# Kernel optimization log

Measured on AMD Instinct MI355X. Metric: run time of the kernel, lower is better.

## Reference

```python
import jax, jax.numpy as jnp
import numpy as np

NUM_HEADS = 8
HEAD_DIM = 64


def setup_inputs() -> dict:
    key = jax.random.key(0)
    k1, k2, k3 = jax.random.split(key, 3)
    B, T, S, D = 2, 32, 1024, 512
    inner = NUM_HEADS * HEAD_DIM  # 512
    x = jax.random.normal(k1, (B, T, S, D), dtype=jnp.float32)
    W_qkv = jax.random.normal(k2, (D, 3 * inner), dtype=jnp.float32) * (D ** -0.5)
    W_out = jax.random.normal(k3, (inner, D), dtype=jnp.float32) * (inner ** -0.5)
    return {"x": x, "W_qkv": W_qkv, "W_out": W_out}


def reference(x, W_qkv, W_out):
    # x: (B, T, S, D); causal attention over T at each spatial position S.
    B, T, S, D = x.shape
    H, hd = NUM_HEADS, HEAD_DIM
    scale = hd ** -0.5
    qkv = jnp.einsum('btsd,de->btse', x, W_qkv)  # (B,T,S,3*H*hd)
    qkv = qkv.reshape(B, T, S, 3, H, hd)
    q, k, v = qkv[..., 0, :, :], qkv[..., 1, :, :], qkv[..., 2, :, :]  # (B,T,S,H,hd)
    # attention logits per (batch, spatial, head): (B,S,H,Tq,Tk)
    attn = jnp.einsum('bqshd,bkshd->bshqk', q, k) * scale
    causal_mask = jnp.triu(jnp.ones((T, T), dtype=bool), 1)  # True above diagonal
    attn = jnp.where(causal_mask, -jnp.inf, attn)
    attn = jax.nn.softmax(attn, axis=-1)
    out = jnp.einsum('bshqk,bkshd->bqshd', attn, v)  # (B,T,S,H,hd)
    out = out.reshape(B, T, S, H * hd)
    return jnp.einsum('btse,ed->btsd', out, W_out)  # (B,T,S,D)
```

## Files before the change

### kernel.cpp

```cpp
#include <hip/hip_runtime.h>
#include <cstdint>
#include <cstddef>

#define KDIM 512

typedef __attribute__((ext_vector_type(8))) __bf16 bf16x8;
typedef __attribute__((ext_vector_type(8))) unsigned short ushort8;
typedef __attribute__((ext_vector_type(4))) float f32x4;
typedef unsigned short u16;

__device__ __forceinline__ float bf2f(u16 u) {
  union { unsigned u32; float f; } x; x.u32 = ((unsigned)u) << 16; return x.f;
}
__device__ __forceinline__ u16 f2bf(float f) {
  union { float f; unsigned u; } x; x.f = f;
  unsigned u = x.u;
  unsigned r = (u + 0x7fffu + ((u >> 16) & 1u)) >> 16;
  return (u16)r;
}

__global__ __launch_bounds__(256) void cast_x_kernel(const float* __restrict__ in,
                                                     u16* __restrict__ out, int n4) {
  int i = blockIdx.x * 256 + threadIdx.x;
  if (i >= n4) return;
  float4 v = ((const float4*)in)[i];
  ushort4 o;
  o.x = f2bf(v.x); o.y = f2bf(v.y); o.z = f2bf(v.z); o.w = f2bf(v.w);
  ((ushort4*)out)[i] = o;
}

__global__ __launch_bounds__(256) void transpose_cast_kernel(const float* __restrict__ in,
                                                             u16* __restrict__ out,
                                                             int R, int C) {
  int o = blockIdx.x * 256 + threadIdx.x;
  if (o >= R * C) return;
  int r = o % R;
  int c = o / R;
  out[o] = f2bf(in[(size_t)r * C + c]);
}

__device__ __forceinline__ void gload_lds16(const void* g, void* l) {
  __builtin_amdgcn_global_load_lds((__attribute__((address_space(1))) unsigned int*)g,
                                   (__attribute__((address_space(3))) unsigned int*)l,
                                   16, 0, 0);
}

template <typename OutT>
__global__ __launch_bounds__(512, 2) void gemm256_kernel(const u16* __restrict__ A,
                                                         const u16* __restrict__ Bt,
                                                         OutT* __restrict__ C,
                                                         int N, int NXT) {
  __shared__ __attribute__((aligned(16))) u16 As[4][8192];
  __shared__ __attribute__((aligned(16))) u16 Bs[4][8192];
  const int tid = threadIdx.x;
  const int wid = tid >> 6, l = tid & 63;
  const int wm = wid >> 2, wn = wid & 3;
  const int g = l >> 4, i = l & 15;

  const int nwg = gridDim.x;
  const int cpx = nwg >> 3;
  const int bid = blockIdx.x;
  const int swz = (bid & 7) * cpx + (bid >> 3);
  const int mt = swz / NXT, nt = swz % NXT;
  const size_t m0 = (size_t)mt * 256, n0 = (size_t)nt * 256;

  const int srow = tid >> 2;
  const int sbp = tid & 3;
  const int sbs = sbp ^ ((srow >> 1) & 3);

  f32x4 acc[8][4] = {};

  auto STAGE = [&](int t, int slot) {
    const int k0 = t << 5;
    gload_lds16(A + (m0 + srow) * KDIM + k0 + sbs * 8, &As[slot][tid * 8]);
    gload_lds16(A + (m0 + 128 + srow) * KDIM + k0 + sbs * 8, &As[slot][(tid + 512) * 8]);
    gload_lds16(Bt + (n0 + srow) * KDIM + k0 + sbs * 8, &Bs[slot][tid * 8]);
    gload_lds16(Bt + (n0 + 128 + srow) * KDIM + k0 + sbs * 8, &Bs[slot][(tid + 512) * 8]);
  };

  auto COMPUTE = [&](int slot) {
    bf16x8 af[8], bv[4];
#pragma unroll
    for (int m = 0; m < 8; ++m) {
      int row = wm * 128 + m * 16 + i;
      af[m] = *(const bf16x8*)&As[slot][row * 32 + ((g ^ ((row >> 1) & 3)) << 3)];
    }
#pragma unroll
    for (int n = 0; n < 4; ++n) {
      int row = wn * 64 + n * 16 + i;
      bv[n] = *(const bf16x8*)&Bs[slot][row * 32 + ((g ^ ((row >> 1) & 3)) << 3)];
    }
    __builtin_amdgcn_s_setprio(1);
#pragma unroll
    for (int m = 0; m < 8; ++m)
#pragma unroll
      for (int n = 0; n < 4; ++n)
        acc[m][n] = __builtin_amdgcn_mfma_f32_16x16x32_bf16(af[m], bv[n], acc[m][n], 0, 0, 0);
    __builtin_amdgcn_s_setprio(0);
  };

  STAGE(0, 0);
  STAGE(1, 1);
  STAGE(2, 2);
  for (int t = 0; t < 14; ++t) {
    asm volatile("s_waitcnt vmcnt(8)" ::: "memory");
    __builtin_amdgcn_s_barrier();
    __builtin_amdgcn_sched_barrier(0);
    if (t < 13) STAGE(t + 3, (t + 3) & 3);
    COMPUTE(t & 3);
    __builtin_amdgcn_sched_barrier(0);
  }
  asm volatile("s_waitcnt vmcnt(4)" ::: "memory");
  __builtin_amdgcn_s_barrier();
  __builtin_amdgcn_sched_barrier(0);
  COMPUTE(2);
  __builtin_amdgcn_sched_barrier(0);
  asm volatile("s_waitcnt vmcnt(0)" ::: "memory");
  __builtin_amdgcn_s_barrier();
  __builtin_amdgcn_sched_barrier(0);
  COMPUTE(3);

#pragma unroll
  for (int m = 0; m < 8; ++m) {
    size_t rowb = m0 + wm * 128 + m * 16 + g * 4;
#pragma unroll
    for (int n = 0; n < 4; ++n) {
      size_t colg = n0 + wn * 64 + n * 16 + i;
#pragma unroll
      for (int r = 0; r < 4; ++r) {
        size_t idx = (rowb + r) * (size_t)N + colg;
        if constexpr (sizeof(OutT) == 2) C[idx] = (OutT)f2bf(acc[m][n][r]);
        else C[idx] = acc[m][n][r];
      }
    }
  }
}

__global__ __launch_bounds__(256, 4) void attn_mfma_kernel(const u16* __restrict__ qkv,
                                                           u16* __restrict__ out) {
  const int bs = blockIdx.x >> 1;
  const int hg = blockIdx.x & 1;
  const int b = bs >> 10, s = bs & 1023;
  __shared__ __attribute__((aligned(16))) u16 Ks[4][2048];
  __shared__ __attribute__((aligned(16))) u16 Vt[4][2048];
  __shared__ __attribute__((aligned(16))) u16 Ps[4][1024];

  const int tid = threadIdx.x;
  const int wv = tid >> 6;
  const int h = hg * 4 + wv;
  const int l = tid & 63;
  const int g = l >> 4, i = l & 15;

  const size_t tstride = (size_t)1024 * 1536;
  const size_t base = ((size_t)(b * 32) * 1024 + s) * 1536;

  {
    const int krow = l >> 3;
    const int dbs = (l & 7) ^ krow;
#pragma unroll
    for (int j = 0; j < 4; ++j) {
      int k = j * 8 + krow;
      gload_lds16(qkv + base + (size_t)k * tstride + 512 + h * 64 + dbs * 8, &Ks[wv][j * 512]);
    }
  }

  const int vk = l & 31;
  ushort8 vv[4];
#pragma unroll
  for (int j = 0; j < 4; ++j) {
    int c = (l >> 5) + 2 * j;
    vv[j] = *(const ushort8*)(qkv + base + (size_t)vk * tstride + 1024 + h * 64 + c * 8);
  }

  bf16x8 bq[2][2];
#pragma unroll
  for (int n = 0; n < 2; ++n)
#pragma unroll
    for (int ks = 0; ks < 2; ++ks)
      bq[n][ks] = *(const bf16x8*)(qkv + base + (size_t)(n * 16 + i) * tstride + h * 64 + ks * 32 + g * 8);

#pragma unroll
  for (int j = 0; j < 4; ++j) {
    int c = (l >> 5) + 2 * j;
#pragma unroll
    for (int u = 0; u < 8; ++u) {
      int d = c * 8 + u;
      int pos = (vk >> 3) ^ (d & 3);
      Vt[wv][d * 32 + pos * 8 + (vk & 7)] = vv[j][u];
    }
  }

  asm volatile("s_waitcnt vmcnt(0)" ::: "memory");

  f32x4 sc[2][2] = {};
#pragma unroll
  for (int m = 0; m < 2; ++m)
#pragma unroll
    for (int ks = 0; ks < 2; ++ks) {
      int k = m * 16 + i;
      int pos = (ks * 4 + g) ^ (k & 7);
      bf16x8 ak = *(const bf16x8*)&Ks[wv][k * 64 + pos * 8];
      sc[m][0] = __builtin_amdgcn_mfma_f32_16x16x32_bf16(ak, bq[0][ks], sc[m][0], 0, 0, 0);
      sc[m][1] = __builtin_amdgcn_mfma_f32_16x16x32_bf16(ak, bq[1][ks], sc[m][1], 0, 0, 0);
    }

  float p[2][2][4];
#pragma unroll
  for (int n = 0; n < 2; ++n) {
    int q = n * 16 + i;
    float m0 = -1e30f;
#pragma unroll
    for (int m = 0; m < 2; ++m)
#pragma unroll
      for (int r = 0; r < 4; ++r) {
        int k = m * 16 + g * 4 + r;
        float v = (k <= q) ? sc[m][n][r] * 0.125f : -1e30f;
        p[m][n][r] = v;
        m0 = fmaxf(m0, v);
      }
    m0 = fmaxf(m0, __shfl_xor(m0, 16));
    m0 = fmaxf(m0, __shfl_xor(m0, 32));
    float s0 = 0.f;
#pragma unroll
    for (int m = 0; m < 2; ++m)
#pragma unroll
      for (int r = 0; r < 4; ++r) {
        float e = __expf(p[m][n][r] - m0);
        p[m][n][r] = e;
        s0 += e;
      }
    s0 += __shfl_xor(s0, 16);
    s0 += __shfl_xor(s0, 32);
    float inv = 1.f / s0;
#pragma unroll
    for (int m = 0; m < 2; ++m)
#pragma unroll
      for (int r = 0; r < 4; ++r) p[m][n][r] *= inv;
  }

#pragma unroll
  for (int m = 0; m < 2; ++m)
#pragma unroll
    for (int n = 0; n < 2; ++n) {
      int q = n * 16 + i;
      int kb = m * 2 + (g >> 1);
      int pos = kb ^ (q & 3);
      uint2 wo;
      wo.x = (unsigned)f2bf(p[m][n][0]) | ((unsigned)f2bf(p[m][n][1]) << 16);
      wo.y = (unsigned)f2bf(p[m][n][2]) | ((unsigned)f2bf(p[m][n][3]) << 16);
      *(uint2*)&Ps[wv][q * 32 + pos * 8 + (g & 1) * 4] = wo;
    }

  asm volatile("s_waitcnt lgkmcnt(0)" ::: "memory");

  bf16x8 bv[4];
#pragma unroll
  for (int np = 0; np < 4; ++np) {
    int d = np * 16 + i;
    int pos = g ^ (d & 3);
    bv[np] = *(const bf16x8*)&Vt[wv][d * 32 + pos * 8];
  }
  f32x4 o[2][4] = {};
#pragma unroll
  for (int mp = 0; mp < 2; ++mp) {
    int q = mp * 16 + i;
    int pos = g ^ (q & 3);
    bf16x8 ap = *(const bf16x8*)&Ps[wv][q * 32 + pos * 8];
#pragma unroll
    for (int np = 0; np < 4; ++np)
      o[mp][np] = __builtin_amdgcn_mfma_f32_16x16x32_bf16(ap, bv[np], o[mp][np], 0, 0, 0);
  }

#pragma unroll
  for (int mp = 0; mp < 2; ++mp)
#pragma unroll
    for (int r = 0; r < 4; ++r) {
      int q = mp * 16 + g * 4 + r;
      u16* dst = out + ((size_t)((b * 32 + q) * 1024 + s)) * 512 + h * 64;
#pragma unroll
      for (int np = 0; np < 4; ++np)
        dst[np * 16 + i] = f2bf(o[mp][np][r]);
    }
}

extern "C" void kernel_launch(void* const* d_in, const int* in_sizes, int n_in,
                              void* d_out, int out_size, void* d_ws, size_t ws_size,
                              hipStream_t stream) {
  const float* x = (const float*)d_in[0];
  const float* Wqkv = (const float*)d_in[1];
  const float* Wout = (const float*)d_in[2];
  float* outp = (float*)d_out;

  char* ws = (char*)d_ws;
  u16* x_bf = (u16*)(ws);
  u16* qkv_bf = (u16*)(ws + (size_t)67108864);
  u16* wqkv_t = (u16*)(ws + (size_t)268435456);
  u16* wout_t = (u16*)(ws + (size_t)270008320);
  u16* attn_o = x_bf;

  cast_x_kernel<<<32768, 256, 0, stream>>>(x, x_bf, 8388608);
  transpose_cast_kernel<<<3072, 256, 0, stream>>>(Wqkv, wqkv_t, 512, 1536);
  transpose_cast_kernel<<<1024, 256, 0, stream>>>(Wout, wout_t, 512, 512);

  gemm256_kernel<u16><<<1536, 512, 0, stream>>>(x_bf, wqkv_t, qkv_bf, 1536, 6);

  attn_mfma_kernel<<<4096, 256, 0, stream>>>(qkv_bf, attn_o);

  gemm256_kernel<float><<<512, 512, 0, stream>>>(attn_o, wout_t, outp, 512, 2);
}
```

Measured before the change: 308.8 us.

## Fuse fp32-to-bf16 cast of x into QKV GEMM and retile output GEMM

```diff
diff --git a/kernel.cpp b/kernel.cpp
--- a/kernel.cpp
+++ b/kernel.cpp
@@ -17,16 +17,6 @@
   unsigned u = x.u;
   unsigned r = (u + 0x7fffu + ((u >> 16) & 1u)) >> 16;
   return (u16)r;
-}
-
-__global__ __launch_bounds__(256) void cast_x_kernel(const float* __restrict__ in,
-                                                     u16* __restrict__ out, int n4) {
-  int i = blockIdx.x * 256 + threadIdx.x;
-  if (i >= n4) return;
-  float4 v = ((const float4*)in)[i];
-  ushort4 o;
-  o.x = f2bf(v.x); o.y = f2bf(v.y); o.z = f2bf(v.z); o.w = f2bf(v.w);
-  ((ushort4*)out)[i] = o;
 }
 
 __global__ __launch_bounds__(256) void transpose_cast_kernel(const float* __restrict__ in,
@@ -45,13 +35,12 @@
                                    16, 0, 0);
 }
 
-template <typename OutT>
-__global__ __launch_bounds__(512, 2) void gemm256_kernel(const u16* __restrict__ A,
-                                                         const u16* __restrict__ Bt,
-                                                         OutT* __restrict__ C,
-                                                         int N, int NXT) {
-  __shared__ __attribute__((aligned(16))) u16 As[4][8192];
-  __shared__ __attribute__((aligned(16))) u16 Bs[4][8192];
+__global__ __launch_bounds__(512, 1) void gemm1f_kernel(const float* __restrict__ X,
+                                                        const u16* __restrict__ Bt,
+                                                        u16* __restrict__ C,
+                                                        int N, int NXT) {
+  __shared__ __attribute__((aligned(16))) u16 As[2][8192];
+  __shared__ __attribute__((aligned(16))) u16 Bs[2][8192];
   const int tid = threadIdx.x;
   const int wid = tid >> 6, l = tid & 63;
   const int wm = wid >> 2, wn = wid & 3;
@@ -64,20 +53,38 @@
   const int mt = swz / NXT, nt = swz % NXT;
   const size_t m0 = (size_t)mt * 256, n0 = (size_t)nt * 256;
 
+  const int ar = tid >> 1, ah = tid & 1;
+  const int asw = (ar >> 1) & 3;
   const int srow = tid >> 2;
   const int sbp = tid & 3;
   const int sbs = sbp ^ ((srow >> 1) & 3);
 
   f32x4 acc[8][4] = {};
-
-  auto STAGE = [&](int t, int slot) {
+  float4 av[4];
+
+  auto LOADA = [&](int t) {
+    const float* src = X + (m0 + ar) * KDIM + (t << 5) + ah * 16;
+#pragma unroll
+    for (int j = 0; j < 4; ++j) av[j] = *(const float4*)(src + j * 4);
+  };
+  auto WRITEA = [&](int slot) {
+#pragma unroll
+    for (int jb = 0; jb < 2; ++jb) {
+      ushort8 w;
+#pragma unroll
+      for (int u = 0; u < 4; ++u) {
+        const float4& v = av[jb * 2 + (u >> 1)];
+        w[u * 2 + 0] = f2bf((u & 1) ? v.z : v.x);
+        w[u * 2 + 1] = f2bf((u & 1) ? v.w : v.y);
+      }
+      *(ushort8*)&As[slot][ar * 32 + (((ah * 2 + jb) ^ asw) << 3)] = w;
+    }
+  };
+  auto STAGEB = [&](int t, int slot) {
     const int k0 = t << 5;
-    gload_lds16(A + (m0 + srow) * KDIM + k0 + sbs * 8, &As[slot][tid * 8]);
-    gload_lds16(A + (m0 + 128 + srow) * KDIM + k0 + sbs * 8, &As[slot][(tid + 512) * 8]);
     gload_lds16(Bt + (n0 + srow) * KDIM + k0 + sbs * 8, &Bs[slot][tid * 8]);
     gload_lds16(Bt + (n0 + 128 + srow) * KDIM + k0 + sbs * 8, &Bs[slot][(tid + 512) * 8]);
   };
-
   auto COMPUTE = [&](int slot) {
     bf16x8 af[8], bv[4];
 #pragma unroll
@@ -99,39 +106,114 @@
     __builtin_amdgcn_s_setprio(0);
   };
 
+  LOADA(0);
+  STAGEB(0, 0);
+  asm volatile("s_waitcnt vmcnt(0)" ::: "memory");
+  WRITEA(0);
+  LOADA(1);
+  asm volatile("s_waitcnt lgkmcnt(0)" ::: "memory");
+  __builtin_amdgcn_s_barrier();
+
+  for (int t = 0; t < 16; ++t) {
+    const int buf = t & 1;
+    if (t < 15) STAGEB(t + 1, buf ^ 1);
+    COMPUTE(buf);
+    if (t < 15) {
+      asm volatile("s_waitcnt vmcnt(0)" ::: "memory");
+      WRITEA(buf ^ 1);
+      if (t < 14) LOADA(t + 2);
+      asm volatile("s_waitcnt lgkmcnt(0)" ::: "memory");
+      __builtin_amdgcn_s_barrier();
+    }
+  }
+
+#pragma unroll
+  for (int m = 0; m < 8; ++m) {
+    size_t rowb = m0 + wm * 128 + m * 16 + g * 4;
+#pragma unroll
+    for (int n = 0; n < 4; ++n) {
+      size_t colg = n0 + wn * 64 + n * 16 + i;
+#pragma unroll
+      for (int r = 0; r < 4; ++r)
+        C[(rowb + r) * (size_t)N + colg] = (u16)f2bf(acc[m][n][r]);
+    }
+  }
+}
+
+__global__ __launch_bounds__(256, 4) void gemm128_kernel(const u16* __restrict__ A,
+                                                         const u16* __restrict__ Bt,
+                                                         float* __restrict__ C,
+                                                         int N, int NXT) {
+  __shared__ __attribute__((aligned(16))) u16 As[2][4096];
+  __shared__ __attribute__((aligned(16))) u16 Bs[2][4096];
+  const int tid = threadIdx.x;
+  const int wid = tid >> 6, l = tid & 63;
+  const int wm = wid >> 1, wn = wid & 1;
+  const int g = l >> 4, i = l & 15;
+
+  const int nwg = gridDim.x;
+  const int cpx = nwg >> 3;
+  const int bid = blockIdx.x;
+  const int swz = (bid & 7) * cpx + (bid >> 3);
+  const int mt = swz / NXT, nt = swz % NXT;
+  const size_t m0 = (size_t)mt * 128, n0 = (size_t)nt * 128;
+
+  f32x4 acc[4][4] = {};
+
+  auto STAGE = [&](int t, int slot) {
+    const int k0 = t << 5;
+#pragma unroll
+    for (int c = 0; c < 2; ++c) {
+      int ch = tid + c * 256;
+      int row = ch >> 2;
+      int bbs = (ch & 3) ^ ((row >> 1) & 3);
+      gload_lds16(A + (m0 + row) * KDIM + k0 + bbs * 8, &As[slot][ch * 8]);
+      gload_lds16(Bt + (n0 + row) * KDIM + k0 + bbs * 8, &Bs[slot][ch * 8]);
+    }
+  };
+  auto COMPUTE = [&](int slot) {
+    bf16x8 af[4], bv[4];
+#pragma unroll
+    for (int m = 0; m < 4; ++m) {
+      int row = wm * 64 + m * 16 + i;
+      af[m] = *(const bf16x8*)&As[slot][row * 32 + ((g ^ ((row >> 1) & 3)) << 3)];
+    }
+#pragma unroll
+    for (int n = 0; n < 4; ++n) {
+      int row = wn * 64 + n * 16 + i;
+      bv[n] = *(const bf16x8*)&Bs[slot][row * 32 + ((g ^ ((row >> 1) & 3)) << 3)];
+    }
+    __builtin_amdgcn_s_setprio(1);
+#pragma unroll
+    for (int m = 0; m < 4; ++m)
+#pragma unroll
+      for (int n = 0; n < 4; ++n)
+        acc[m][n] = __builtin_amdgcn_mfma_f32_16x16x32_bf16(af[m], bv[n], acc[m][n], 0, 0, 0);
+    __builtin_amdgcn_s_setprio(0);
+  };
+
   STAGE(0, 0);
-  STAGE(1, 1);
-  STAGE(2, 2);
-  for (int t = 0; t < 14; ++t) {
-    asm volatile("s_waitcnt vmcnt(8)" ::: "memory");
-    __builtin_amdgcn_s_barrier();
-    __builtin_amdgcn_sched_barrier(0);
-    if (t < 13) STAGE(t + 3, (t + 3) & 3);
-    COMPUTE(t & 3);
-    __builtin_amdgcn_sched_barrier(0);
-  }
-  asm volatile("s_waitcnt vmcnt(4)" ::: "memory");
-  __builtin_amdgcn_s_barrier();
-  __builtin_amdgcn_sched_barrier(0);
-  COMPUTE(2);
-  __builtin_amdgcn_sched_barrier(0);
   asm volatile("s_waitcnt vmcnt(0)" ::: "memory");
   __builtin_amdgcn_s_barrier();
-  __builtin_amdgcn_sched_barrier(0);
-  COMPUTE(3);
-
-#pragma unroll
-  for (int m = 0; m < 8; ++m) {
-    size_t rowb = m0 + wm * 128 + m * 16 + g * 4;
+  for (int t = 0; t < 16; ++t) {
+    const int buf = t & 1;
+    if (t < 15) STAGE(t + 1, buf ^ 1);
+    COMPUTE(buf);
+    if (t < 15) {
+      asm volatile("s_waitcnt vmcnt(0)" ::: "memory");
+      __builtin_amdgcn_s_barrier();
+    }
+  }
+
+#pragma unroll
+  for (int m = 0; m < 4; ++m) {
+    size_t rowb = m0 + wm * 64 + m * 16 + g * 4;
 #pragma unroll
     for (int n = 0; n < 4; ++n) {
       size_t colg = n0 + wn * 64 + n * 16 + i;
 #pragma unroll
-      for (int r = 0; r < 4; ++r) {
-        size_t idx = (rowb + r) * (size_t)N + colg;
-        if constexpr (sizeof(OutT) == 2) C[idx] = (OutT)f2bf(acc[m][n][r]);
-        else C[idx] = acc[m][n][r];
-      }
+      for (int r = 0; r < 4; ++r)
+        C[(rowb + r) * (size_t)N + colg] = acc[m][n][r];
     }
   }
 }
@@ -292,19 +374,17 @@
   float* outp = (float*)d_out;
 
   char* ws = (char*)d_ws;
-  u16* x_bf = (u16*)(ws);
+  u16* attn_o = (u16*)(ws);
   u16* qkv_bf = (u16*)(ws + (size_t)67108864);
   u16* wqkv_t = (u16*)(ws + (size_t)268435456);
   u16* wout_t = (u16*)(ws + (size_t)270008320);
-  u16* attn_o = x_bf;
-
-  cast_x_kernel<<<32768, 256, 0, stream>>>(x, x_bf, 8388608);
+
   transpose_cast_kernel<<<3072, 256, 0, stream>>>(Wqkv, wqkv_t, 512, 1536);
   transpose_cast_kernel<<<1024, 256, 0, stream>>>(Wout, wout_t, 512, 512);
 
-  gemm256_kernel<u16><<<1536, 512, 0, stream>>>(x_bf, wqkv_t, qkv_bf, 1536, 6);
+  gemm1f_kernel<<<1536, 512, 0, stream>>>(x, wqkv_t, qkv_bf, 1536, 6);
 
   attn_mfma_kernel<<<4096, 256, 0, stream>>>(qkv_bf, attn_o);
 
-  gemm256_kernel<float><<<512, 512, 0, stream>>>(attn_o, wout_t, outp, 512, 2);
-}
+  gemm128_kernel<<<2048, 256, 0, stream>>>(attn_o, wout_t, outp, 512, 4);
+}
```

Measured after the change: 336.3 us. 1.09x slower.

## Replace 256x256 four-stage GEMM with 128x128 double-buffered GEMM

Applied to the files above, without the earlier changes.

```diff
diff --git a/kernel.cpp b/kernel.cpp
--- a/kernel.cpp
+++ b/kernel.cpp
@@ -46,15 +46,15 @@
 }
 
 template <typename OutT>
-__global__ __launch_bounds__(512, 2) void gemm256_kernel(const u16* __restrict__ A,
+__global__ __launch_bounds__(256, 4) void gemm128_kernel(const u16* __restrict__ A,
                                                          const u16* __restrict__ Bt,
                                                          OutT* __restrict__ C,
                                                          int N, int NXT) {
-  __shared__ __attribute__((aligned(16))) u16 As[4][8192];
-  __shared__ __attribute__((aligned(16))) u16 Bs[4][8192];
+  __shared__ __attribute__((aligned(16))) u16 As[2][4096];
+  __shared__ __attribute__((aligned(16))) u16 Bs[2][4096];
   const int tid = threadIdx.x;
   const int wid = tid >> 6, l = tid & 63;
-  const int wm = wid >> 2, wn = wid & 3;
+  const int wm = wid >> 1, wn = wid & 1;
   const int g = l >> 4, i = l & 15;
 
   const int nwg = gridDim.x;
@@ -62,27 +62,26 @@
   const int bid = blockIdx.x;
   const int swz = (bid & 7) * cpx + (bid >> 3);
   const int mt = swz / NXT, nt = swz % NXT;
-  const size_t m0 = (size_t)mt * 256, n0 = (size_t)nt * 256;
-
-  const int srow = tid >> 2;
-  const int sbp = tid & 3;
-  const int sbs = sbp ^ ((srow >> 1) & 3);
-
-  f32x4 acc[8][4] = {};
+  const size_t m0 = (size_t)mt * 128, n0 = (size_t)nt * 128;
+
+  f32x4 acc[4][4] = {};
 
   auto STAGE = [&](int t, int slot) {
     const int k0 = t << 5;
-    gload_lds16(A + (m0 + srow) * KDIM + k0 + sbs * 8, &As[slot][tid * 8]);
-    gload_lds16(A + (m0 + 128 + srow) * KDIM + k0 + sbs * 8, &As[slot][(tid + 512) * 8]);
-    gload_lds16(Bt + (n0 + srow) * KDIM + k0 + sbs * 8, &Bs[slot][tid * 8]);
-    gload_lds16(Bt + (n0 + 128 + srow) * KDIM + k0 + sbs * 8, &Bs[slot][(tid + 512) * 8]);
+#pragma unroll
+    for (int c = 0; c < 2; ++c) {
+      int ch = tid + c * 256;
+      int row = ch >> 2;
+      int bbs = (ch & 3) ^ ((row >> 1) & 3);
+      gload_lds16(A + (m0 + row) * KDIM + k0 + bbs * 8, &As[slot][ch * 8]);
+      gload_lds16(Bt + (n0 + row) * KDIM + k0 + bbs * 8, &Bs[slot][ch * 8]);
+    }
   };
-
   auto COMPUTE = [&](int slot) {
-    bf16x8 af[8], bv[4];
-#pragma unroll
-    for (int m = 0; m < 8; ++m) {
-      int row = wm * 128 + m * 16 + i;
+    bf16x8 af[4], bv[4];
+#pragma unroll
+    for (int m = 0; m < 4; ++m) {
+      int row = wm * 64 + m * 16 + i;
       af[m] = *(const bf16x8*)&As[slot][row * 32 + ((g ^ ((row >> 1) & 3)) << 3)];
     }
 #pragma unroll
@@ -92,7 +91,7 @@
     }
     __builtin_amdgcn_s_setprio(1);
 #pragma unroll
-    for (int m = 0; m < 8; ++m)
+    for (int m = 0; m < 4; ++m)
 #pragma unroll
       for (int n = 0; n < 4; ++n)
         acc[m][n] = __builtin_amdgcn_mfma_f32_16x16x32_bf16(af[m], bv[n], acc[m][n], 0, 0, 0);
@@ -100,29 +99,21 @@
   };
 
   STAGE(0, 0);
-  STAGE(1, 1);
-  STAGE(2, 2);
-  for (int t = 0; t < 14; ++t) {
-    asm volatile("s_waitcnt vmcnt(8)" ::: "memory");
-    __builtin_amdgcn_s_barrier();
-    __builtin_amdgcn_sched_barrier(0);
-    if (t < 13) STAGE(t + 3, (t + 3) & 3);
-    COMPUTE(t & 3);
-    __builtin_amdgcn_sched_barrier(0);
-  }
-  asm volatile("s_waitcnt vmcnt(4)" ::: "memory");
-  __builtin_amdgcn_s_barrier();
-  __builtin_amdgcn_sched_barrier(0);
-  COMPUTE(2);
-  __builtin_amdgcn_sched_barrier(0);
   asm volatile("s_waitcnt vmcnt(0)" ::: "memory");
   __builtin_amdgcn_s_barrier();
-  __builtin_amdgcn_sched_barrier(0);
-  COMPUTE(3);
-
-#pragma unroll
-  for (int m = 0; m < 8; ++m) {
-    size_t rowb = m0 + wm * 128 + m * 16 + g * 4;
+  for (int t = 0; t < 16; ++t) {
+    const int buf = t & 1;
+    if (t < 15) STAGE(t + 1, buf ^ 1);
+    COMPUTE(buf);
+    if (t < 15) {
+      asm volatile("s_waitcnt vmcnt(0)" ::: "memory");
+      __builtin_amdgcn_s_barrier();
+    }
+  }
+
+#pragma unroll
+  for (int m = 0; m < 4; ++m) {
+    size_t rowb = m0 + wm * 64 + m * 16 + g * 4;
 #pragma unroll
     for (int n = 0; n < 4; ++n) {
       size_t colg = n0 + wn * 64 + n * 16 + i;
@@ -302,9 +293,9 @@
   transpose_cast_kernel<<<3072, 256, 0, stream>>>(Wqkv, wqkv_t, 512, 1536);
   transpose_cast_kernel<<<1024, 256, 0, stream>>>(Wout, wout_t, 512, 512);
 
-  gemm256_kernel<u16><<<1536, 512, 0, stream>>>(x_bf, wqkv_t, qkv_bf, 1536, 6);
+  gemm128_kernel<u16><<<6144, 256, 0, stream>>>(x_bf, wqkv_t, qkv_bf, 1536, 12);
 
   attn_mfma_kernel<<<4096, 256, 0, stream>>>(qkv_bf, attn_o);
 
-  gemm256_kernel<float><<<512, 512, 0, stream>>>(attn_o, wout_t, outp, 512, 2);
-}
+  gemm128_kernel<float><<<2048, 256, 0, stream>>>(attn_o, wout_t, outp, 512, 4);
+}
```

Result: no change. 304.9 us (-1.3%).

## Fuse attention with output projection in one kernel per spatial position

Applied to the files above, without the earlier changes.

```diff
diff --git a/kernel.cpp b/kernel.cpp
--- a/kernel.cpp
+++ b/kernel.cpp
@@ -45,10 +45,9 @@
                                    16, 0, 0);
 }
 
-template <typename OutT>
 __global__ __launch_bounds__(512, 2) void gemm256_kernel(const u16* __restrict__ A,
                                                          const u16* __restrict__ Bt,
-                                                         OutT* __restrict__ C,
+                                                         u16* __restrict__ C,
                                                          int N, int NXT) {
   __shared__ __attribute__((aligned(16))) u16 As[4][8192];
   __shared__ __attribute__((aligned(16))) u16 Bs[4][8192];
@@ -127,27 +126,23 @@
     for (int n = 0; n < 4; ++n) {
       size_t colg = n0 + wn * 64 + n * 16 + i;
 #pragma unroll
-      for (int r = 0; r < 4; ++r) {
-        size_t idx = (rowb + r) * (size_t)N + colg;
-        if constexpr (sizeof(OutT) == 2) C[idx] = (OutT)f2bf(acc[m][n][r]);
-        else C[idx] = acc[m][n][r];
-      }
-    }
-  }
-}
-
-__global__ __launch_bounds__(256, 4) void attn_mfma_kernel(const u16* __restrict__ qkv,
-                                                           u16* __restrict__ out) {
-  const int bs = blockIdx.x >> 1;
-  const int hg = blockIdx.x & 1;
+      for (int r = 0; r < 4; ++r)
+        C[(rowb + r) * (size_t)N + colg] = f2bf(acc[m][n][r]);
+    }
+  }
+}
+
+__global__ __launch_bounds__(512, 4) void attn_out_kernel(const u16* __restrict__ qkv,
+                                                          const u16* __restrict__ wout_t,
+                                                          float* __restrict__ outp) {
+  const int bs = blockIdx.x;
   const int b = bs >> 10, s = bs & 1023;
-  __shared__ __attribute__((aligned(16))) u16 Ks[4][2048];
-  __shared__ __attribute__((aligned(16))) u16 Vt[4][2048];
-  __shared__ __attribute__((aligned(16))) u16 Ps[4][1024];
+  __shared__ __attribute__((aligned(16))) u16 Ks[8][2048];
+  __shared__ __attribute__((aligned(16))) u16 Vt[8][2048];
 
   const int tid = threadIdx.x;
   const int wv = tid >> 6;
-  const int h = hg * 4 + wv;
+  const int h = wv;
   const int l = tid & 63;
   const int g = l >> 4, i = l & 15;
 
@@ -238,6 +233,7 @@
       for (int r = 0; r < 4; ++r) p[m][n][r] *= inv;
   }
 
+  u16* Psw = &Ks[wv][0];
 #pragma unroll
   for (int m = 0; m < 2; ++m)
 #pragma unroll
@@ -248,27 +244,27 @@
       uint2 wo;
       wo.x = (unsigned)f2bf(p[m][n][0]) | ((unsigned)f2bf(p[m][n][1]) << 16);
       wo.y = (unsigned)f2bf(p[m][n][2]) | ((unsigned)f2bf(p[m][n][3]) << 16);
-      *(uint2*)&Ps[wv][q * 32 + pos * 8 + (g & 1) * 4] = wo;
+      *(uint2*)&Psw[q * 32 + pos * 8 + (g & 1) * 4] = wo;
     }
 
   asm volatile("s_waitcnt lgkmcnt(0)" ::: "memory");
 
-  bf16x8 bv[4];
+  bf16x8 bvf[4];
 #pragma unroll
   for (int np = 0; np < 4; ++np) {
     int d = np * 16 + i;
     int pos = g ^ (d & 3);
-    bv[np] = *(const bf16x8*)&Vt[wv][d * 32 + pos * 8];
+    bvf[np] = *(const bf16x8*)&Vt[wv][d * 32 + pos * 8];
   }
   f32x4 o[2][4] = {};
 #pragma unroll
   for (int mp = 0; mp < 2; ++mp) {
     int q = mp * 16 + i;
     int pos = g ^ (q & 3);
-    bf16x8 ap = *(const bf16x8*)&Ps[wv][q * 32 + pos * 8];
+    bf16x8 ap = *(const bf16x8*)&Psw[q * 32 + pos * 8];
 #pragma unroll
     for (int np = 0; np < 4; ++np)
-      o[mp][np] = __builtin_amdgcn_mfma_f32_16x16x32_bf16(ap, bv[np], o[mp][np], 0, 0, 0);
+      o[mp][np] = __builtin_amdgcn_mfma_f32_16x16x32_bf16(ap, bvf[np], o[mp][np], 0, 0, 0);
   }
 
 #pragma unroll
@@ -276,10 +272,45 @@
 #pragma unroll
     for (int r = 0; r < 4; ++r) {
       int q = mp * 16 + g * 4 + r;
-      u16* dst = out + ((size_t)((b * 32 + q) * 1024 + s)) * 512 + h * 64;
-#pragma unroll
-      for (int np = 0; np < 4; ++np)
-        dst[np * 16 + i] = f2bf(o[mp][np][r]);
+#pragma unroll
+      for (int np = 0; np < 4; ++np) {
+        int d = np * 16 + i;
+        Vt[wv][q * 64 + ((((d >> 3)) ^ (q & 7)) << 3) + (d & 7)] = f2bf(o[mp][np][r]);
+      }
+    }
+
+  __syncthreads();
+
+  f32x4 acc2[2][4] = {};
+#pragma unroll 4
+  for (int ks = 0; ks < 16; ++ks) {
+    bf16x8 af2[2];
+#pragma unroll
+    for (int mf = 0; mf < 2; ++mf) {
+      int q = mf * 16 + i;
+      int dblk = (ks & 1) * 4 + g;
+      af2[mf] = *(const bf16x8*)&Vt[ks >> 1][q * 64 + ((dblk ^ (q & 7)) << 3)];
+    }
+    bf16x8 bw[4];
+#pragma unroll
+    for (int n = 0; n < 4; ++n)
+      bw[n] = *(const bf16x8*)(wout_t + (size_t)(wv * 64 + n * 16 + i) * 512 + ks * 32 + g * 8);
+#pragma unroll
+    for (int mf = 0; mf < 2; ++mf)
+#pragma unroll
+      for (int n = 0; n < 4; ++n)
+        acc2[mf][n] = __builtin_amdgcn_mfma_f32_16x16x32_bf16(af2[mf], bw[n], acc2[mf][n], 0, 0, 0);
+  }
+
+#pragma unroll
+  for (int mf = 0; mf < 2; ++mf)
+#pragma unroll
+    for (int r = 0; r < 4; ++r) {
+      int q = mf * 16 + g * 4 + r;
+      float* dst = outp + ((size_t)((b * 32 + q) * 1024 + s)) * 512 + wv * 64;
+#pragma unroll
+      for (int n = 0; n < 4; ++n)
+        dst[n * 16 + i] = acc2[mf][n][r];
     }
 }
 
@@ -296,15 +327,12 @@
   u16* qkv_bf = (u16*)(ws + (size_t)67108864);
   u16* wqkv_t = (u16*)(ws + (size_t)268435456);
   u16* wout_t = (u16*)(ws + (size_t)270008320);
-  u16* attn_o = x_bf;
 
   cast_x_kernel<<<32768, 256, 0, stream>>>(x, x_bf, 8388608);
   transpose_cast_kernel<<<3072, 256, 0, stream>>>(Wqkv, wqkv_t, 512, 1536);
   transpose_cast_kernel<<<1024, 256, 0, stream>>>(Wout, wout_t, 512, 512);
 
-  gemm256_kernel<u16><<<1536, 512, 0, stream>>>(x_bf, wqkv_t, qkv_bf, 1536, 6);
-
-  attn_mfma_kernel<<<4096, 256, 0, stream>>>(qkv_bf, attn_o);
-
-  gemm256_kernel<float><<<512, 512, 0, stream>>>(attn_o, wout_t, outp, 512, 2);
-}
+  gemm256_kernel<<<1536, 512, 0, stream>>>(x_bf, wqkv_t, qkv_bf, 1536, 6);
+
+  attn_out_kernel<<<2048, 512, 0, stream>>>(qkv_bf, wout_t, outp);
+}
```

Measured after the change: 344.4 us. 11.5% more time.
